# Optimization experiments

Hardware: AMD Instinct MI355X
Metric: run time of the kernel (lower is better)

Reference implementation:

```python
import jax, jax.numpy as jnp
import numpy as np

B, N, H = 4, 200, 300


def setup_inputs() -> dict:
    key = jax.random.key(0)
    ks = jax.random.split(key, 6)
    s = 1.0 / np.sqrt(H)
    return {
        "x": jax.random.normal(ks[0], (B, N, H), dtype=jnp.float32),
        "e": jax.random.normal(ks[1], (B, N, N, H), dtype=jnp.float32),
        "U_w": jax.random.uniform(ks[2], (H, H), jnp.float32, -s, s),
        "U_b": jax.random.uniform(ks[3], (H,), jnp.float32, -s, s),
        "V_w": jax.random.uniform(ks[4], (H, H), jnp.float32, -s, s),
        "V_b": jax.random.uniform(ks[5], (H,), jnp.float32, -s, s),
    }


def reference(x, e, U_w, U_b, V_w, V_b):
    # Ue = e @ U_w.T + U_b  -> (B, N, N, H)
    Ue = jnp.einsum("bijh,gh->bijg", e, U_w) + U_b
    # Vx = x @ V_w.T + V_b  -> (B, N, H)
    Vx = jnp.einsum("bnh,gh->bng", x, V_w) + V_b
    # e_new[b,i,j] = Ue[b,i,j] + Vx[b,i] + Vx[b,j]
    e_new = Ue + Vx[:, :, None, :] + Vx[:, None, :, :]
    return e_new
```

## Files before the change

### kernel.cpp

```cpp
#include <hip/hip_runtime.h>
#include <hip/hip_bf16.h>

#define BB 4
#define NN 200
#define HH 300
#define GF 20
#define BM 64

typedef __attribute__((ext_vector_type(8))) short short8;
typedef __attribute__((ext_vector_type(4))) float float4v;

static __device__ __forceinline__ ushort f2bf(float x) {
    union { float f; uint u; } v; v.f = x;
    uint r = v.u + 0x7FFFu + ((v.u >> 16) & 1u);
    return (ushort)(r >> 16);
}

static __device__ __forceinline__ short8 pack8_cvt(float4v a, float4v b) {
    uint u0, u1, u2, u3;
    asm("v_cvt_pk_bf16_f32 %0, %1, %2" : "=v"(u0) : "v"(a[0]), "v"(a[1]));
    asm("v_cvt_pk_bf16_f32 %0, %1, %2" : "=v"(u1) : "v"(a[2]), "v"(a[3]));
    asm("v_cvt_pk_bf16_f32 %0, %1, %2" : "=v"(u2) : "v"(b[0]), "v"(b[1]));
    asm("v_cvt_pk_bf16_f32 %0, %1, %2" : "=v"(u3) : "v"(b[2]), "v"(b[3]));
    union { uint u[4]; short8 s; } r;
    r.u[0] = u0; r.u[1] = u1; r.u[2] = u2; r.u[3] = u3;
    return r.s;
}

static __device__ __forceinline__ void gload_lds16(const void* g, void* l) {
    __builtin_amdgcn_global_load_lds(
        (const __attribute__((address_space(1))) unsigned int*)g,
        (__attribute__((address_space(3))) unsigned int*)l, 16, 0, 0);
}

__global__ void pack_u(const float* __restrict__ Uw, ushort* __restrict__ Bp) {
    int idx = blockIdx.x * 256 + threadIdx.x;
    if (idx >= 10 * GF * 64) return;
    int lane = idx & 63;
    int kg = idx >> 6;
    int gf = kg % GF, ks = kg / GF;
    int g = gf * 16 + (lane & 15);
    int h0 = ks * 32 + (lane >> 4) * 8;
    ushort v[8];
#pragma unroll
    for (int j = 0; j < 8; ++j) {
        int h = h0 + j;
        v[j] = (g < HH && h < HH) ? f2bf(Uw[g * HH + h]) : (ushort)0;
    }
    *reinterpret_cast<short8*>(Bp + (size_t)idx * 8) = *reinterpret_cast<const short8*>(v);
}

__global__ void vx_kernel(const float* __restrict__ x, const float* __restrict__ Vw,
                          const float* __restrict__ Vb, const float* __restrict__ Ub,
                          float* __restrict__ Vx) {
    __shared__ float xs[HH];
    int row = blockIdx.x;
    const float* xr = x + (size_t)row * HH;
    for (int h = threadIdx.x; h < HH; h += 256) xs[h] = xr[h];
    __syncthreads();
    for (int g = threadIdx.x; g < HH; g += 256) {
        const float4* wr = reinterpret_cast<const float4*>(Vw + (size_t)g * HH);
        const float4* xv = reinterpret_cast<const float4*>(xs);
        float s0 = 0.f, s1 = 0.f, s2 = 0.f, s3 = 0.f;
#pragma unroll 5
        for (int k = 0; k < HH / 4; ++k) {
            float4 w = wr[k];
            float4 xx = xv[k];
            s0 += w.x * xx.x; s1 += w.y * xx.y; s2 += w.z * xx.z; s3 += w.w * xx.w;
        }
        Vx[(size_t)row * HH + g] = Vb[g] + 0.5f * Ub[g] + s0 + s1 + s2 + s3;
    }
}

__launch_bounds__(256, 2)
__global__ void gemm_kernel(const float* __restrict__ e, const ushort* __restrict__ Bp,
                            const float* __restrict__ Vx, float* __restrict__ out) {
    __shared__ __align__(16) ushort Blds[2][20480];
    const int tid = threadIdx.x;
    const int w = tid >> 6, l = tid & 63;
    const int r = l & 15, q = l >> 4;
    const int m0 = blockIdx.x * BM;
    const float* rowp = e + (size_t)(m0 + w * 16 + r) * HH;

    float4v acc[GF];
#pragma unroll
    for (int f = 0; f < GF; ++f) acc[f] = (float4v){0.f, 0.f, 0.f, 0.f};

    float4v s0a0, s0a1, s0b0, s0b1, s1a0, s1a1, s1b0, s1b1;

#define LOAD_A(KC_, S_) do {                                                    \
        int ca_ = (KC_) * 64 + q * 8;                                           \
        int cb_ = ca_ + 32;                                                     \
        const float* pa0_ = (ca_ + 4 <= HH) ? rowp + ca_ : e;                   \
        const float* pa1_ = (ca_ + 8 <= HH) ? rowp + ca_ + 4 : e;               \
        const float* pb0_ = (cb_ + 4 <= HH) ? rowp + cb_ : e;                   \
        const float* pb1_ = (cb_ + 8 <= HH) ? rowp + cb_ + 4 : e;               \
        S_##a0 = *reinterpret_cast<const float4v*>(pa0_);                       \
        S_##a1 = *reinterpret_cast<const float4v*>(pa1_);                       \
        S_##b0 = *reinterpret_cast<const float4v*>(pb0_);                       \
        S_##b1 = *reinterpret_cast<const float4v*>(pb1_);                       \
    } while (0)

#define STAGE_B(KC_, P_) do {                                                   \
        const char* bs_ = (const char*)Bp + (size_t)(KC_) * 40960;              \
        char* bd_ = (char*)&Blds[P_][0];                                        \
        _Pragma("unroll")                                                       \
        for (int rd_ = 0; rd_ < 10; ++rd_)                                      \
            gload_lds16(bs_ + rd_ * 4096 + tid * 16, bd_ + rd_ * 4096 + tid * 16); \
    } while (0)

#define COMPUTE(KC_, P_, S_) do {                                               \
        short8 fa0_ = pack8_cvt(S_##a0, S_##a1);                                \
        short8 fa1_ = pack8_cvt(S_##b0, S_##b1);                                \
        if ((KC_) == 4) {          \
            int c0_ = 288 + q * 8;                                              \
            _Pragma("unroll")                                                   \
            for (int j_ = 0; j_ < 8; ++j_)                                      \
                if (c0_ + j_ >= HH) fa1_[j_] = 0;                               \
        }                                                                       \
        const ushort* bb_ = &Blds[P_][l * 8];                                   \
        _Pragma("unroll")                                                       \
        for (int f_ = 0; f_ < GF; ++f_) {                                       \
            short8 bf_ = *reinterpret_cast<const short8*>(bb_ + f_ * 512);      \
            acc[f_] = __builtin_amdgcn_mfma_f32_16x16x32_bf16(bf_, fa0_, acc[f_], 0, 0, 0); \
        }                                                                       \
        _Pragma("unroll")                                                       \
        for (int f_ = 0; f_ < GF; ++f_) {                                       \
            short8 bf_ = *reinterpret_cast<const short8*>(bb_ + 10240 + f_ * 512); \
            acc[f_] = __builtin_amdgcn_mfma_f32_16x16x32_bf16(bf_, fa1_, acc[f_], 0, 0, 0); \
        }                                                                       \
    } while (0)

#define WAITV(N_) do {                                                          \
        __builtin_amdgcn_sched_barrier(0);                                      \
        asm volatile("s_waitcnt vmcnt(" #N_ ")" ::: "memory");                  \
        __builtin_amdgcn_sched_barrier(0);                                      \
    } while (0)

#define BARX() do {                                                             \
        asm volatile("s_waitcnt lgkmcnt(0)" ::: "memory");                      \
        __builtin_amdgcn_s_barrier();                                           \
        __builtin_amdgcn_sched_barrier(0);                                      \
    } while (0)

    STAGE_B(0, 0); LOAD_A(0, s0);
    STAGE_B(1, 1); LOAD_A(1, s1);
    WAITV(14); BARX();

    COMPUTE(0, 0, s0); BARX();
    STAGE_B(2, 0); LOAD_A(2, s0); WAITV(14); BARX();
    COMPUTE(1, 1, s1); BARX();
    STAGE_B(3, 1); LOAD_A(3, s1); WAITV(14); BARX();
    COMPUTE(2, 0, s0); BARX();
    STAGE_B(4, 0); LOAD_A(4, s0); WAITV(14); BARX();
    COMPUTE(3, 1, s1); BARX();
    WAITV(0); BARX();
    COMPUTE(4, 0, s0);

    {
        const int m = m0 + w * 16 + r;
        int j = m % NN;
        int ti = m / NN;
        int b = ti / NN;
        const float* vi = Vx + (size_t)ti * HH;
        const float* vj = Vx + (size_t)(b * NN + j) * HH;
        float* orow = out + (size_t)m * HH;
#pragma unroll
        for (int f = 0; f < GF - 1; ++f) {
            int g0 = f * 16 + q * 4;
            if (g0 + 4 <= HH) {
                float4v vi4 = *reinterpret_cast<const float4v*>(vi + g0);
                float4v vj4 = *reinterpret_cast<const float4v*>(vj + g0);
                *reinterpret_cast<float4v*>(orow + g0) = acc[f] + vi4 + vj4;
            }
        }
    }
#undef LOAD_A
#undef STAGE_B
#undef COMPUTE
#undef WAITV
#undef BARX
}

extern "C" void kernel_launch(void* const* d_in, const int* in_sizes, int n_in,
                              void* d_out, int out_size, void* d_ws, size_t ws_size,
                              hipStream_t stream) {
    const float* x  = (const float*)d_in[0];
    const float* e  = (const float*)d_in[1];
    const float* Uw = (const float*)d_in[2];
    const float* Ub = (const float*)d_in[3];
    const float* Vw = (const float*)d_in[4];
    const float* Vb = (const float*)d_in[5];
    float* out = (float*)d_out;

    ushort* Bp = (ushort*)d_ws;
    float*  Vx = (float*)((char*)d_ws + 204800);

    pack_u<<<50, 256, 0, stream>>>(Uw, Bp);
    vx_kernel<<<BB * NN, 256, 0, stream>>>(x, Vw, Vb, Ub, Vx);
    gemm_kernel<<<160000 / BM, 256, 0, stream>>>(e, Bp, Vx, out);
}
```

Before: 151.6 us.

## Use 512-thread GEMM blocks with 128 rows and batch four rows per Vx block

The GEMM block grows to 128 rows and 512 threads, so each staged bf16 U tile in LDS is shared by eight waves instead of four. Each thread now issues half as many LDS-staging loads, and the vmcnt waits are adjusted to match. The Vx kernel computes four x rows per block, reusing each Vw row load four times and using a quarter of the blocks. The costs are fewer GEMM workgroups (1250) and possible occupancy limits from the larger block size.

New measurement: 156.0 us. +2.9%, slower.

```diff
diff --git a/kernel.cpp b/kernel.cpp
--- a/kernel.cpp
+++ b/kernel.cpp
@@ -5,7 +5,7 @@
 #define NN 200
 #define HH 300
 #define GF 20
-#define BM 64
+#define BM 128
 
 typedef __attribute__((ext_vector_type(8))) short short8;
 typedef __attribute__((ext_vector_type(4))) float float4v;
@@ -53,26 +53,39 @@
 __global__ void vx_kernel(const float* __restrict__ x, const float* __restrict__ Vw,
                           const float* __restrict__ Vb, const float* __restrict__ Ub,
                           float* __restrict__ Vx) {
-    __shared__ float xs[HH];
-    int row = blockIdx.x;
-    const float* xr = x + (size_t)row * HH;
-    for (int h = threadIdx.x; h < HH; h += 256) xs[h] = xr[h];
+    __shared__ __align__(16) float xs[4][304];
+    const int tid = threadIdx.x;
+    const int row0 = blockIdx.x * 4;
+    for (int i = tid; i < 300; i += 256) {
+        int rr = i / 75, c = (i % 75) * 4;
+        *reinterpret_cast<float4v*>(&xs[rr][c]) =
+            *reinterpret_cast<const float4v*>(x + (size_t)(row0 + rr) * HH + c);
+    }
     __syncthreads();
-    for (int g = threadIdx.x; g < HH; g += 256) {
-        const float4* wr = reinterpret_cast<const float4*>(Vw + (size_t)g * HH);
-        const float4* xv = reinterpret_cast<const float4*>(xs);
-        float s0 = 0.f, s1 = 0.f, s2 = 0.f, s3 = 0.f;
+    for (int g = tid; g < HH; g += 256) {
+        const float4v* wr = reinterpret_cast<const float4v*>(Vw + (size_t)g * HH);
+        float a0 = 0.f, a1 = 0.f, a2 = 0.f, a3 = 0.f;
 #pragma unroll 5
-        for (int k = 0; k < HH / 4; ++k) {
-            float4 w = wr[k];
-            float4 xx = xv[k];
-            s0 += w.x * xx.x; s1 += w.y * xx.y; s2 += w.z * xx.z; s3 += w.w * xx.w;
+        for (int k = 0; k < 75; ++k) {
+            float4v w = wr[k];
+            float4v x0 = *reinterpret_cast<const float4v*>(&xs[0][k * 4]);
+            float4v x1 = *reinterpret_cast<const float4v*>(&xs[1][k * 4]);
+            float4v x2 = *reinterpret_cast<const float4v*>(&xs[2][k * 4]);
+            float4v x3 = *reinterpret_cast<const float4v*>(&xs[3][k * 4]);
+            a0 += w[0]*x0[0] + w[1]*x0[1] + w[2]*x0[2] + w[3]*x0[3];
+            a1 += w[0]*x1[0] + w[1]*x1[1] + w[2]*x1[2] + w[3]*x1[3];
+            a2 += w[0]*x2[0] + w[1]*x2[1] + w[2]*x2[2] + w[3]*x2[3];
+            a3 += w[0]*x3[0] + w[1]*x3[1] + w[2]*x3[2] + w[3]*x3[3];
         }
-        Vx[(size_t)row * HH + g] = Vb[g] + 0.5f * Ub[g] + s0 + s1 + s2 + s3;
-    }
-}
-
-__launch_bounds__(256, 2)
+        float bias = Vb[g] + 0.5f * Ub[g];
+        Vx[(size_t)(row0 + 0) * HH + g] = bias + a0;
+        Vx[(size_t)(row0 + 1) * HH + g] = bias + a1;
+        Vx[(size_t)(row0 + 2) * HH + g] = bias + a2;
+        Vx[(size_t)(row0 + 3) * HH + g] = bias + a3;
+    }
+}
+
+__launch_bounds__(512, 2)
 __global__ void gemm_kernel(const float* __restrict__ e, const ushort* __restrict__ Bp,
                             const float* __restrict__ Vx, float* __restrict__ out) {
     __shared__ __align__(16) ushort Blds[2][20480];
@@ -105,8 +118,8 @@
         const char* bs_ = (const char*)Bp + (size_t)(KC_) * 40960;              \
         char* bd_ = (char*)&Blds[P_][0];                                        \
         _Pragma("unroll")                                                       \
-        for (int rd_ = 0; rd_ < 10; ++rd_)                                      \
-            gload_lds16(bs_ + rd_ * 4096 + tid * 16, bd_ + rd_ * 4096 + tid * 16); \
+        for (int rd_ = 0; rd_ < 5; ++rd_)                                       \
+            gload_lds16(bs_ + rd_ * 8192 + tid * 16, bd_ + rd_ * 8192 + tid * 16); \
     } while (0)
 
 #define COMPUTE(KC_, P_, S_) do {                                               \
@@ -145,14 +158,14 @@
 
     STAGE_B(0, 0); LOAD_A(0, s0);
     STAGE_B(1, 1); LOAD_A(1, s1);
-    WAITV(14); BARX();
+    WAITV(9); BARX();
 
     COMPUTE(0, 0, s0); BARX();
-    STAGE_B(2, 0); LOAD_A(2, s0); WAITV(14); BARX();
+    STAGE_B(2, 0); LOAD_A(2, s0); WAITV(9); BARX();
     COMPUTE(1, 1, s1); BARX();
-    STAGE_B(3, 1); LOAD_A(3, s1); WAITV(14); BARX();
+    STAGE_B(3, 1); LOAD_A(3, s1); WAITV(9); BARX();
     COMPUTE(2, 0, s0); BARX();
-    STAGE_B(4, 0); LOAD_A(4, s0); WAITV(14); BARX();
+    STAGE_B(4, 0); LOAD_A(4, s0); WAITV(9); BARX();
     COMPUTE(3, 1, s1); BARX();
     WAITV(0); BARX();
     COMPUTE(4, 0, s0);
@@ -197,6 +210,6 @@
     float*  Vx = (float*)((char*)d_ws + 204800);
 
     pack_u<<<50, 256, 0, stream>>>(Uw, Bp);
-    vx_kernel<<<BB * NN, 256, 0, stream>>>(x, Vw, Vb, Ub, Vx);
-    gemm_kernel<<<160000 / BM, 256, 0, stream>>>(e, Bp, Vx, out);
-}
+    vx_kernel<<<200, 256, 0, stream>>>(x, Vw, Vb, Ub, Vx);
+    gemm_kernel<<<160000 / BM, 512, 0, stream>>>(e, Bp, Vx, out);
+}
```
